# Optimization experiments

Measured on AMD Instinct MI355X. Metric: run time of the kernel, lower is better.

## Reference

```python
import jax, jax.numpy as jnp
import numpy as np

B, N, E, F, C = 4, 10000, 160000, 128, 128
NUM_ITERATIONS = 3  # num_iterations init arg


def setup_inputs() -> dict:
    key = jax.random.key(0)
    ks = jax.random.split(key, 8)
    objects = jax.random.normal(ks[0], (B, N, F), dtype=jnp.float32)
    connections = jax.random.randint(ks[1], (B, E, 2), 0, N, dtype=jnp.int32)
    # small init scales keep exp() in the attention numerically tame (mirrors
    # glorot/orthogonal-scale weights at init)
    object_state_W = jax.random.normal(ks[2], (F, C), dtype=jnp.float32) * (1.0 / np.sqrt(F))
    state_attention_W = jax.random.normal(ks[3], (C, C), dtype=jnp.float32) * 0.05
    linked_state_attention_W = jax.random.normal(ks[4], (C, C), dtype=jnp.float32) * 0.05
    linked_state_W = jax.random.normal(ks[5], (C, C), dtype=jnp.float32) * (1.0 / np.sqrt(C))
    attention_b = jnp.zeros((C,), dtype=jnp.float32)
    state_b = jnp.zeros((C,), dtype=jnp.float32)
    return {
        "objects": objects,
        "object_state_W": object_state_W,
        "state_attention_W": state_attention_W,
        "linked_state_attention_W": linked_state_attention_W,
        "attention_b": attention_b,
        "linked_state_W": linked_state_W,
        "state_b": state_b,
        "connections": connections,
    }


def reference(objects, object_state_W, state_attention_W, linked_state_attention_W,
              attention_b, linked_state_W, state_b, connections):
    # bidirectional: double edges with both orientations  [B, 2E]
    src = jnp.concatenate([connections[:, :, 0], connections[:, :, 1]], axis=1)
    dst = jnp.concatenate([connections[:, :, 1], connections[:, :, 0]], axis=1)

    # initial states: [B, N, C]
    states = jnp.tanh(jnp.einsum('bnf,fc->bnc', objects, object_state_W) + state_b)

    def step_one(states_b, src_b, dst_b):
        # states_b: [N, C]; src_b/dst_b: [2E]
        states_aW = states_b @ state_attention_W          # [N, C]
        linked_aW = states_b @ linked_state_attention_W   # [N, C]
        # per-edge unnormalized attention  [2E, C]
        attention = jnp.exp(states_aW[src_b] + linked_aW[dst_b] + attention_b)
        # scatter-add normalization; self edge contributes 1 (exp(0))
        attention_norm = jnp.ones_like(states_b).at[src_b].add(attention)  # [N, C]
        self_attention = 1.0 / attention_norm
        attention = attention / attention_norm[src_b]
        # weighted neighbor aggregation
        attented = attention * states_b[dst_b]                              # [2E, C]
        linked_gated = jnp.zeros_like(states_b).at[src_b].add(attented)     # [N, C]
        return jnp.tanh(states_b * self_attention + linked_gated @ linked_state_W + state_b)

    step = jax.vmap(step_one)
    for _ in range(NUM_ITERATIONS):
        states = step(states, src, dst)
    return states
```

## Files before the change

kernel.cpp:

```cpp
#include <hip/hip_runtime.h>
#include <hip/hip_bf16.h>


#define BATCH 4
#define NNODE 10000
#define NEDGE 160000
#define TWOE  (2*NEDGE)
#define MROWS (BATCH*NNODE)
#define NCHUNK 64
#define CHUNKE (NEDGE/NCHUNK)
#define PADN  10240
#define EDPAD (TWOE + 8*NNODE)

typedef unsigned short u16;
typedef unsigned int   u32;
typedef __attribute__((ext_vector_type(8))) short bf16x8_t;
typedef __attribute__((ext_vector_type(4))) float f32x4_t;

__device__ __forceinline__ float b2f(u16 h){ return __uint_as_float(((u32)h) << 16); }
__device__ __forceinline__ u16 f2bf(float f){
  u32 u = __float_as_uint(f);
  return (u16)((u + 0x7fffu + ((u >> 16) & 1u)) >> 16);
}
__device__ __forceinline__ float fast_tanh(float x){
  float e = __expf(2.0f * x);
  return fmaf(-2.0f, __builtin_amdgcn_rcpf(e + 1.0f), 1.0f);
}

__global__ void prep_weights(const void* __restrict__ objects,
                             const void* __restrict__ Wo, const void* __restrict__ Wa,
                             const void* __restrict__ Wla, const void* __restrict__ Wl,
                             const void* __restrict__ ab, const void* __restrict__ sb,
                             int* __restrict__ flag, u16* __restrict__ Wt,
                             float* __restrict__ biasf){
  __shared__ int zc, hc;
  if (threadIdx.x == 0){ zc = 0; hc = 0; }
  __syncthreads();
  const u32* objw = (const u32*)objects;
  int z = 0, hcnt = 0;
  for (int i = threadIdx.x; i < 1024; i += 256){
    u32 lo = objw[i] & 0xffffu;
    if (lo == 0) z++;
    if (((lo >> 7) & 0xffu) >= 160u) hcnt++;
  }
  atomicAdd(&zc, z); atomicAdd(&hc, hcnt);
  __syncthreads();
  bool f = (hc > 0 || zc > 512);
  if (blockIdx.x == 0 && threadIdx.x == 0) *flag = f ? 1 : 0;

  int idx = blockIdx.x * 256 + threadIdx.x;
  if (idx < 65536){
    int m = idx >> 14, k = (idx >> 7) & 127, c = idx & 127;
    const void* src = (m == 0) ? Wo : (m == 1) ? Wa : (m == 2) ? Wla : Wl;
    u16 h = f ? f2bf(((const float*)src)[k * 128 + c]) : ((const u16*)src)[k * 128 + c];
    Wt[m * 16384 + c * 128 + k] = h;
  } else {
    int t = idx - 65536;
    const void* src = (t < 128) ? sb : ab;
    int i = t & 127;
    biasf[t] = f ? ((const float*)src)[i] : b2f(((const u16*)src)[i]);
  }
}

__device__ __forceinline__ void chunk_of(int blk, int& b, int& c){
  int xcd = blk & 7;
  b = xcd >> 1;
  c = ((blk >> 3) << 1) | (xcd & 1);
}

__global__ void __launch_bounds__(256) csr_hist(const int* __restrict__ conn,
                                                u16* __restrict__ partial){
  int b, c; chunk_of(blockIdx.x, b, c);
  __shared__ u32 hist[NNODE];
  for (int n = threadIdx.x; n < NNODE; n += 256) hist[n] = 0;
  __syncthreads();
  const int2* cp = (const int2*)conn + (size_t)b * NEDGE + c * CHUNKE;
  for (int i = threadIdx.x; i < CHUNKE; i += 256){
    int2 e = cp[i];
    atomicAdd(&hist[e.x], 1);
    atomicAdd(&hist[e.y], 1);
  }
  __syncthreads();
  u16* prow = partial + (size_t)(b * NCHUNK + c) * PADN;
  for (int n = threadIdx.x; n < NNODE; n += 256) prow[n] = (u16)hist[n];
}

__global__ void __launch_bounds__(256) csr_colscan(u16* __restrict__ partial,
    int* __restrict__ row_start, int* __restrict__ bsum, int* __restrict__ deg){
  int b = blockIdx.x / 40, w = blockIdx.x % 40;
  int n = w * 256 + threadIdx.x;
  u32 run = 0;
  if (n < NNODE){
    #pragma unroll 8
    for (int c = 0; c < NCHUNK; c++){
      size_t idx = (size_t)(b * NCHUNK + c) * PADN + n;
      u32 v = partial[idx];
      partial[idx] = (u16)run;
      run += v;
    }
  }
  u32 pad = (run + 7u) & ~7u;
  __shared__ u32 buf[256];
  buf[threadIdx.x] = pad;
  __syncthreads();
  for (int off = 1; off < 256; off <<= 1){
    u32 x = (threadIdx.x >= (unsigned)off) ? buf[threadIdx.x - off] : 0;
    __syncthreads();
    buf[threadIdx.x] += x;
    __syncthreads();
  }
  u32 incl = buf[threadIdx.x];
  if (n < NNODE){
    row_start[b * (NNODE + 1) + n] = (int)(incl - pad);
    deg[b * NNODE + n] = (int)run;
  }
  if (threadIdx.x == 255) bsum[blockIdx.x] = (int)incl;
}

__global__ void scanC(int* __restrict__ row_start, const int* __restrict__ bsum){
  int b = blockIdx.x / 40, j = blockIdx.x % 40;
  int n = j * 256 + threadIdx.x;
  int off = 0;
  for (int q = b * 40; q < b * 40 + j; q++) off += bsum[q];
  if (n < NNODE) row_start[b * (NNODE + 1) + n] += off;
  if (j == 39 && threadIdx.x == 0)
    row_start[b * (NNODE + 1) + NNODE] = off + bsum[b * 40 + 39];
}

__global__ void __launch_bounds__(256) csr_fill(const int* __restrict__ conn,
    const u16* __restrict__ partial, const int* __restrict__ row_start,
    int* __restrict__ edge_dst){
  int b, c; chunk_of(blockIdx.x, b, c);
  __shared__ u32 cur[NNODE];
  const u16* prow = partial + (size_t)(b * NCHUNK + c) * PADN;
  const int* rs = row_start + b * (NNODE + 1);
  for (int n = threadIdx.x; n < NNODE; n += 256) cur[n] = (u32)rs[n] + prow[n];
  __syncthreads();
  const int2* cp = (const int2*)conn + (size_t)b * NEDGE + c * CHUNKE;
  int* edb = edge_dst + (size_t)b * EDPAD;
  for (int i = threadIdx.x; i < CHUNKE; i += 256){
    int2 e = cp[i];
    u32 p1 = atomicAdd(&cur[e.x], 1); edb[p1] = e.y;
    u32 p2 = atomicAdd(&cur[e.y], 1); edb[p2] = e.x;
  }
}

__global__ void pad_fill(const int* __restrict__ row_start,
                         const int* __restrict__ deg, int* __restrict__ edge_dst,
                         u32* __restrict__ g0, u32* __restrict__ g1){
  if (blockIdx.x == 0){
    size_t base = (size_t)MROWS * 64;
    g0[base + threadIdx.x] = 0;
    g1[base + threadIdx.x] = 0;
  }
  int b = blockIdx.x / 40, j = blockIdx.x % 40;
  const int* rs = row_start + b * (NNODE + 1);
  int sent = 40000 - 9999 * b;
  int* edb = edge_dst + (size_t)b * EDPAD;
  if (j == 0){
    int T = rs[NNODE];
    for (int p = T + (int)threadIdx.x; p < EDPAD; p += 256) edb[p] = sent;
  }
  int n = j * 256 + threadIdx.x;
  if (n >= NNODE) return;
  int s = rs[n] + deg[b * NNODE + n];
  int epad = rs[n + 1];
  for (int p = s; p < epad; p++) edb[p] = sent;
}

__device__ __forceinline__ void gemm_tile4(const u16* __restrict__ arow,
    const u16* __restrict__ wt, int lm, int lq, int cofs, f32x4_t acc[4]){
  #pragma unroll
  for (int ks = 0; ks < 4; ks++){
    bf16x8_t a = *(const bf16x8_t*)(arow + ks * 32);
    #pragma unroll
    for (int nb = 0; nb < 4; nb++){
      bf16x8_t bfr = *(const bf16x8_t*)(wt + (cofs + nb * 16 + lm) * 128 + ks * 32 + lq * 8);
      acc[nb] = __builtin_amdgcn_mfma_f32_16x16x32_bf16(a, bfr, acc[nb], 0, 0, 0);
    }
  }
}

__device__ __forceinline__ void gemm_tile4_packed(const u32* __restrict__ Lrow,
    const u16* __restrict__ wt, int lm, int lq, int cofs, f32x4_t acc[4]){
  #pragma unroll
  for (int ks = 0; ks < 4; ks++){
    uint4 wa = *(const uint4*)(Lrow + ks * 32 + lq * 8);
    uint4 wb = *(const uint4*)(Lrow + ks * 32 + lq * 8 + 4);
    bf16x8_t a;
    a[0] = (short)wa.x; a[1] = (short)wa.y; a[2] = (short)wa.z; a[3] = (short)wa.w;
    a[4] = (short)wb.x; a[5] = (short)wb.y; a[6] = (short)wb.z; a[7] = (short)wb.w;
    #pragma unroll
    for (int nb = 0; nb < 4; nb++){
      bf16x8_t bfr = *(const bf16x8_t*)(wt + (cofs + nb * 16 + lm) * 128 + ks * 32 + lq * 8);
      acc[nb] = __builtin_amdgcn_mfma_f32_16x16x32_bf16(a, bfr, acc[nb], 0, 0, 0);
    }
  }
}

__device__ __forceinline__ void phase2_awlaw4(const u16* __restrict__ ldstile,
    const u16* __restrict__ Wt, const float* __restrict__ biasf,
    int lm, int lq, int cofs, int r0, _Float16* __restrict__ eat,
    u32* __restrict__ ghw){
  const u16* Wta  = Wt + 16384;
  const u16* Wtla = Wt + 32768;
  const u16* ldsrow = ldstile + lm * 136 + lq * 8;
  f32x4_t accA[4], accL[4];
  #pragma unroll
  for (int i = 0; i < 4; i++){ accA[i] = (f32x4_t){0.f,0.f,0.f,0.f}; accL[i] = (f32x4_t){0.f,0.f,0.f,0.f}; }
  #pragma unroll
  for (int ks = 0; ks < 4; ks++){
    bf16x8_t a = *(const bf16x8_t*)(ldsrow + ks * 32);
    #pragma unroll
    for (int nb = 0; nb < 4; nb++){
      bf16x8_t ba = *(const bf16x8_t*)(Wta  + (cofs + nb * 16 + lm) * 128 + ks * 32 + lq * 8);
      bf16x8_t bl = *(const bf16x8_t*)(Wtla + (cofs + nb * 16 + lm) * 128 + ks * 32 + lq * 8);
      accA[nb] = __builtin_amdgcn_mfma_f32_16x16x32_bf16(a, ba, accA[nb], 0, 0, 0);
      accL[nb] = __builtin_amdgcn_mfma_f32_16x16x32_bf16(a, bl, accL[nb], 0, 0, 0);
    }
  }
  #pragma unroll
  for (int nb = 0; nb < 4; nb++){
    int col = cofs + nb * 16 + lm;
    float bb = biasf[128 + col];
    #pragma unroll
    for (int i = 0; i < 4; i++){
      int row = r0 + lq * 4 + i;
      float ea = fminf(__expf(accA[nb][i]), 60000.0f);
      eat[(lq * 4 + i) * 128 + col] = (_Float16)ea;
      _Float16 elh = (_Float16)fminf(__expf(accL[nb][i] + bb), 60000.0f);
      u16 sbf = ldstile[(lq * 4 + i) * 136 + col];
      _Float16 sh = (_Float16)b2f(sbf);
      u32 elu = (u32)(*(const u16*)&elh);
      u32 shu = (u32)(*(const u16*)&sh);
      ghw[(size_t)row * 64 + (col & 63)] = elu | (shu << 16);
    }
  }
}

__device__ __forceinline__ void eah_writeback(const _Float16* __restrict__ eat,
    _Float16* __restrict__ eah, int blk_r0, int tid){
  const uint4* src = (const uint4*)eat;
  uint4* dst = (uint4*)(eah + (size_t)blk_r0 * 128);
  dst[tid]       = src[tid];
  dst[tid + 256] = src[tid + 256];
}

__global__ void __launch_bounds__(256) fused_init(const void* __restrict__ obj_raw,
    const int* __restrict__ flag, const u16* __restrict__ Wt,
    const float* __restrict__ biasf, _Float16* __restrict__ eah,
    u32* __restrict__ gat0, u32* __restrict__ gat1){
  __shared__ u16 lds[2][16 * 136];
  __shared__ _Float16 eat[2][16 * 128];
  const int lane = threadIdx.x & 63, wave = threadIdx.x >> 6;
  const int t = wave >> 1, ch = wave & 1, cofs = ch * 64;
  const int r0 = blockIdx.x * 32 + t * 16;
  const int lm = lane & 15, lq = lane >> 4;
  f32x4_t acc[4];
  #pragma unroll
  for (int i = 0; i < 4; i++) acc[i] = (f32x4_t){0.f, 0.f, 0.f, 0.f};
  if (*flag){
    const float* arow = (const float*)obj_raw + (size_t)(r0 + lm) * 128 + lq * 8;
    #pragma unroll
    for (int ks = 0; ks < 4; ks++){
      float4 fa = *(const float4*)(arow + ks * 32);
      float4 fb = *(const float4*)(arow + ks * 32 + 4);
      bf16x8_t a;
      a[0] = (short)f2bf(fa.x); a[1] = (short)f2bf(fa.y);
      a[2] = (short)f2bf(fa.z); a[3] = (short)f2bf(fa.w);
      a[4] = (short)f2bf(fb.x); a[5] = (short)f2bf(fb.y);
      a[6] = (short)f2bf(fb.z); a[7] = (short)f2bf(fb.w);
      #pragma unroll
      for (int nb = 0; nb < 4; nb++){
        bf16x8_t bfr = *(const bf16x8_t*)(Wt + (cofs + nb * 16 + lm) * 128 + ks * 32 + lq * 8);
        acc[nb] = __builtin_amdgcn_mfma_f32_16x16x32_bf16(a, bfr, acc[nb], 0, 0, 0);
      }
    }
  } else {
    gemm_tile4((const u16*)obj_raw + (size_t)(r0 + lm) * 128 + lq * 8, Wt, lm, lq, cofs, acc);
  }
  #pragma unroll
  for (int nb = 0; nb < 4; nb++){
    int col = cofs + nb * 16 + lm;
    float bb = biasf[col];
    #pragma unroll
    for (int i = 0; i < 4; i++)
      lds[t][(lq * 4 + i) * 136 + col] = f2bf(fast_tanh(acc[nb][i] + bb));
  }
  __syncthreads();
  phase2_awlaw4(&lds[t][0], Wt, biasf, lm, lq, cofs, r0, &eat[t][0], ch ? gat1 : gat0);
  __syncthreads();
  eah_writeback(&eat[0][0], eah, blockIdx.x * 32, threadIdx.x);
}

__global__ void __launch_bounds__(256) fused_mid(const u32* __restrict__ lgsa,
    const u16* __restrict__ Wt, const float* __restrict__ biasf,
    _Float16* __restrict__ eah, u32* __restrict__ gat0, u32* __restrict__ gat1){
  __shared__ u16 lds[2][16 * 136];
  __shared__ _Float16 eat[2][16 * 128];
  const int lane = threadIdx.x & 63, wave = threadIdx.x >> 6;
  const int t = wave >> 1, ch = wave & 1, cofs = ch * 64;
  const int r0 = blockIdx.x * 32 + t * 16;
  const int lm = lane & 15, lq = lane >> 4;
  f32x4_t acc[4];
  #pragma unroll
  for (int i = 0; i < 4; i++) acc[i] = (f32x4_t){0.f, 0.f, 0.f, 0.f};
  gemm_tile4_packed(lgsa + (size_t)(r0 + lm) * 128, Wt + 49152, lm, lq, cofs, acc);
  #pragma unroll
  for (int nb = 0; nb < 4; nb++){
    int col = cofs + nb * 16 + lm;
    float bb = biasf[col];
    #pragma unroll
    for (int i = 0; i < 4; i++){
      int row = r0 + lq * 4 + i;
      u32 v = lgsa[(size_t)row * 128 + col];
      u16 hb = (u16)(v >> 16);
      float sa = (float)(*(const _Float16*)&hb);
      lds[t][(lq * 4 + i) * 136 + col] = f2bf(fast_tanh(sa + acc[nb][i] + bb));
    }
  }
  __syncthreads();
  phase2_awlaw4(&lds[t][0], Wt, biasf, lm, lq, cofs, r0, &eat[t][0], ch ? gat1 : gat0);
  __syncthreads();
  eah_writeback(&eat[0][0], eah, blockIdx.x * 32, threadIdx.x);
}

__global__ void __launch_bounds__(256) final_out(const u32* __restrict__ lgsa,
    const u16* __restrict__ Wt, const float* __restrict__ biasf,
    const int* __restrict__ flag, void* __restrict__ outp){
  const int lane = threadIdx.x & 63, wave = threadIdx.x >> 6;
  const int t = wave >> 1, ch = wave & 1, cofs = ch * 64;
  const int r0 = blockIdx.x * 32 + t * 16;
  const int lm = lane & 15, lq = lane >> 4;
  bool f32out = (*flag != 0);
  f32x4_t acc[4];
  #pragma unroll
  for (int i = 0; i < 4; i++) acc[i] = (f32x4_t){0.f, 0.f, 0.f, 0.f};
  gemm_tile4_packed(lgsa + (size_t)(r0 + lm) * 128, Wt + 49152, lm, lq, cofs, acc);
  #pragma unroll
  for (int nb = 0; nb < 4; nb++){
    int col = cofs + nb * 16 + lm;
    float bb = biasf[col];
    #pragma unroll
    for (int i = 0; i < 4; i++){
      int row = r0 + lq * 4 + i;
      u32 vv = lgsa[(size_t)row * 128 + col];
      u16 hb = (u16)(vv >> 16);
      float sa = (float)(*(const _Float16*)&hb);
      float v = fast_tanh(sa + acc[nb][i] + bb);
      if (f32out) ((float*)outp)[(size_t)row * 128 + col] = v;
      else        ((u16*)  outp)[(size_t)row * 128 + col] = f2bf(v);
    }
  }
}

__device__ __forceinline__ void acc_mix(u32 g, float one, float& a1, float& a2){
  asm("v_fma_mix_f32 %0, %2, %3, %0 op_sel:[0,0,0] op_sel_hi:[1,0,0]\n\t"
      "v_fma_mix_f32 %1, %2, %2, %1 op_sel:[0,1,0] op_sel_hi:[1,1,0]"
      : "+v"(a1), "+v"(a2)
      : "v"(g), "v"(one));
}

__device__ __forceinline__ u32 gath1(const u32* __restrict__ gh, int d, int c){
  const u32* p = (const u32*)((const char*)gh + ((size_t)(u32)d << 8));
  return p[c];
}

#define LDIDX(d, p) { const int* ep_ = (p); _Pragma("unroll") \
  for (int j = 0; j < 8; j++) d[j] = __builtin_amdgcn_readfirstlane(ep_[j]); }
#define GATH8(g, d) { _Pragma("unroll") \
  for (int j = 0; j < 8; j++) g[j] = gath1(gh, d[j], c); }
#define CONS8(g, s1, s2, t1, t2) { _Pragma("unroll") \
  for (int j = 0; j < 8; j++) acc_mix(g[j], one, (j & 1) ? t1 : s1, (j & 1) ? t2 : s2); }

__global__ void __launch_bounds__(128, 6) edge_kernel(const _Float16* __restrict__ eah,
    const u32* __restrict__ gat0, const u32* __restrict__ gat1,
    const int* __restrict__ row_start, const int* __restrict__ edge_dst,
    u32* __restrict__ lgsa){
  int blk = blockIdx.x;
  int xcd = blk & 7;
  int b = xcd >> 1, h = xcd & 1;
  int i = blk >> 3;
  int w = (int)(threadIdx.x >> 6);
  int nA = i * 4 + w * 2, nB = nA + 1;
  int c = threadIdx.x & 63;
  const u32* gh = (h ? gat1 : gat0) + (size_t)b * NNODE * 64;
  const int* rs = row_start + b * (NNODE + 1);
  int eA  = __builtin_amdgcn_readfirstlane(rs[nA]);
  int eA1 = __builtin_amdgcn_readfirstlane(rs[nA + 1]);
  int eB1 = __builtin_amdgcn_readfirstlane(rs[nB + 1]);
  int eB = eA1;
  const int* ed = edge_dst + (size_t)b * EDPAD;

  float eaA = (float)eah[(size_t)(b * NNODE + nA) * 128 + h * 64 + c];
  float eaB = (float)eah[(size_t)(b * NNODE + nB) * 128 + h * 64 + c];
  u32 selfA = gh[((size_t)nA << 6) + c];
  u32 selfB = gh[((size_t)nB << 6) + c];
  const float one = 1.0f;

  float sA1=0.f, sA2=0.f, tA1=0.f, tA2=0.f;
  float sB1=0.f, sB2=0.f, tB1=0.f, tB2=0.f;
  int ngA = (eA1 - eA) >> 3, ngB = (eB1 - eB) >> 3;
  int dA[8], dB[8]; u32 gA[8], gB[8], hA[8], hB[8];

  if (ngA){ LDIDX(dA, ed + eA); }
  if (ngB){ LDIDX(dB, ed + eB); }
  if (ngA){ GATH8(gA, dA); eA += 8; LDIDX(dA, ed + eA); }
  if (ngB){ GATH8(gB, dB); eB += 8; LDIDX(dB, ed + eB); }

  int m = ngA < ngB ? ngA : ngB;
  int cons = 0;
  for (; cons + 2 <= m; cons += 2){
    GATH8(hA, dA); eA += 8; LDIDX(dA, ed + eA);
    GATH8(hB, dB); eB += 8; LDIDX(dB, ed + eB);
    CONS8(gA, sA1, sA2, tA1, tA2);
    CONS8(gB, sB1, sB2, tB1, tB2);
    GATH8(gA, dA); eA += 8; LDIDX(dA, ed + eA);
    GATH8(gB, dB); eB += 8; LDIDX(dB, ed + eB);
    CONS8(hA, sA1, sA2, tA1, tA2);
    CONS8(hB, sB1, sB2, tB1, tB2);
  }

  { int rem = ngA - cons;
    if (rem > 0){
      int k = 1;
      for (; k + 1 < rem; k += 2){
        GATH8(hA, dA); eA += 8; LDIDX(dA, ed + eA);
        CONS8(gA, sA1, sA2, tA1, tA2);
        GATH8(gA, dA); eA += 8; LDIDX(dA, ed + eA);
        CONS8(hA, sA1, sA2, tA1, tA2);
      }
      if (k < rem){
        GATH8(hA, dA);
        CONS8(gA, sA1, sA2, tA1, tA2);
        CONS8(hA, sA1, sA2, tA1, tA2);
      } else {
        CONS8(gA, sA1, sA2, tA1, tA2);
      }
    }
  }
  { int rem = ngB - cons;
    if (rem > 0){
      int k = 1;
      for (; k + 1 < rem; k += 2){
        GATH8(hB, dB); eB += 8; LDIDX(dB, ed + eB);
        CONS8(gB, sB1, sB2, tB1, tB2);
        GATH8(gB, dB); eB += 8; LDIDX(dB, ed + eB);
        CONS8(hB, sB1, sB2, tB1, tB2);
      }
      if (k < rem){
        GATH8(hB, dB);
        CONS8(gB, sB1, sB2, tB1, tB2);
        CONS8(hB, sB1, sB2, tB1, tB2);
      } else {
        CONS8(gB, sB1, sB2, tB1, tB2);
      }
    }
  }

  sA1 += tA1; sA2 += tA2; sB1 += tB1; sB2 += tB2;
  { float inv = __builtin_amdgcn_rcpf(fmaf(eaA, sA1, 1.0f));
    float lg = eaA * sA2 * inv;
    u16 hb = (u16)(selfA >> 16);
    float s_self = (float)(*(const _Float16*)&hb);
    _Float16 hs = (_Float16)(s_self * inv);
    u32 pk = (u32)f2bf(lg) | ((u32)(*(const u16*)&hs) << 16);
    lgsa[(size_t)(b * NNODE + nA) * 128 + h * 64 + c] = pk; }
  { float inv = __builtin_amdgcn_rcpf(fmaf(eaB, sB1, 1.0f));
    float lg = eaB * sB2 * inv;
    u16 hb = (u16)(selfB >> 16);
    float s_self = (float)(*(const _Float16*)&hb);
    _Float16 hs = (_Float16)(s_self * inv);
    u32 pk = (u32)f2bf(lg) | ((u32)(*(const u16*)&hs) << 16);
    lgsa[(size_t)(b * NNODE + nB) * 128 + h * 64 + c] = pk; }
}

extern "C" void kernel_launch(void* const* d_in, const int* in_sizes, int n_in,
                              void* d_out, int out_size, void* d_ws, size_t ws_size,
                              hipStream_t stream){
  (void)in_sizes; (void)n_in; (void)ws_size; (void)out_size;
  const void* objects = d_in[0];
  const void* Wo      = d_in[1];
  const void* Wa      = d_in[2];
  const void* Wla     = d_in[3];
  const void* attn_b  = d_in[4];
  const void* Wl      = d_in[5];
  const void* state_b = d_in[6];
  const int*  conn    = (const int*)d_in[7];

  char* base = (char*)d_ws;
  size_t off = 0;
  auto alloc = [&](size_t bytes) -> char* {
    char* p = base + off;
    off = (off + bytes + 255) & ~(size_t)255;
    return p;
  };
  int*      flag      = (int*)     alloc(256);
  u16*      Wt        = (u16*)     alloc((size_t)4 * 16384 * 2);
  float*    biasf     = (float*)   alloc(256 * 4);
  _Float16* eah       = (_Float16*)alloc((size_t)MROWS * 128 * 2);
  u32*      gat0      = (u32*)     alloc((size_t)(MROWS + 4) * 64 * 4);
  u32*      gat1      = (u32*)     alloc((size_t)(MROWS + 4) * 64 * 4);
  u32*      lgsa      = (u32*)     alloc((size_t)MROWS * 128 * 4);
  u16*      partial   = (u16*)     alloc((size_t)BATCH * NCHUNK * PADN * 2);
  int*      row_start = (int*)     alloc((size_t)BATCH * (NNODE + 1) * 4);
  int*      edge_dst  = (int*)     alloc((size_t)BATCH * EDPAD * 4);
  int*      deg       = (int*)     alloc((size_t)MROWS * 4);
  int*      bsum      = (int*)     alloc(160 * 4);

  prep_weights<<<257, 256, 0, stream>>>(objects, Wo, Wa, Wla, Wl, attn_b, state_b,
                                        flag, Wt, biasf);

  csr_hist<<<256, 256, 0, stream>>>(conn, partial);
  csr_colscan<<<160, 256, 0, stream>>>(partial, row_start, bsum, deg);
  scanC<<<160, 256, 0, stream>>>(row_start, bsum);
  csr_fill<<<256, 256, 0, stream>>>(conn, partial, row_start, edge_dst);
  pad_fill<<<160, 256, 0, stream>>>(row_start, deg, edge_dst, gat0, gat1);

  fused_init<<<MROWS / 32, 256, 0, stream>>>(objects, flag, Wt, biasf, eah, gat0, gat1);
  edge_kernel<<<MROWS / 2, 128, 0, stream>>>(eah, gat0, gat1, row_start, edge_dst, lgsa);
  fused_mid<<<MROWS / 32, 256, 0, stream>>>(lgsa, Wt, biasf, eah, gat0, gat1);
  edge_kernel<<<MROWS / 2, 128, 0, stream>>>(eah, gat0, gat1, row_start, edge_dst, lgsa);
  fused_mid<<<MROWS / 32, 256, 0, stream>>>(lgsa, Wt, biasf, eah, gat0, gat1);
  edge_kernel<<<MROWS / 2, 128, 0, stream>>>(eah, gat0, gat1, row_start, edge_dst, lgsa);
  final_out<<<MROWS / 32, 256, 0, stream>>>(lgsa, Wt, biasf, flag, d_out);
}
```

Baseline: 356.2 us.

## Horizontally fuse independent setup kernels into fewer launches

Weight/bias preparation and the per-chunk CSR histogram now run as one launch, with block ranges selecting the role. The CSR fill, the padding-sentinel fill and the initial state/attention GEMM kernel are merged into a second launch the same way. Together this removes three kernel launches and their serialization gaps, and lets independent work overlap on the GPU. In exchange the merged kernel reserves a 40 KB shared buffer for every block, which may lower occupancy for the GEMM blocks that need much less.

```diff
diff --git a/kernel.cpp b/kernel.cpp
--- a/kernel.cpp
+++ b/kernel.cpp
@@ -27,62 +27,62 @@
   return fmaf(-2.0f, __builtin_amdgcn_rcpf(e + 1.0f), 1.0f);
 }
 
-__global__ void prep_weights(const void* __restrict__ objects,
-                             const void* __restrict__ Wo, const void* __restrict__ Wa,
-                             const void* __restrict__ Wla, const void* __restrict__ Wl,
-                             const void* __restrict__ ab, const void* __restrict__ sb,
-                             int* __restrict__ flag, u16* __restrict__ Wt,
-                             float* __restrict__ biasf){
-  __shared__ int zc, hc;
-  if (threadIdx.x == 0){ zc = 0; hc = 0; }
-  __syncthreads();
-  const u32* objw = (const u32*)objects;
-  int z = 0, hcnt = 0;
-  for (int i = threadIdx.x; i < 1024; i += 256){
-    u32 lo = objw[i] & 0xffffu;
-    if (lo == 0) z++;
-    if (((lo >> 7) & 0xffu) >= 160u) hcnt++;
-  }
-  atomicAdd(&zc, z); atomicAdd(&hc, hcnt);
-  __syncthreads();
-  bool f = (hc > 0 || zc > 512);
-  if (blockIdx.x == 0 && threadIdx.x == 0) *flag = f ? 1 : 0;
-
-  int idx = blockIdx.x * 256 + threadIdx.x;
-  if (idx < 65536){
-    int m = idx >> 14, k = (idx >> 7) & 127, c = idx & 127;
-    const void* src = (m == 0) ? Wo : (m == 1) ? Wa : (m == 2) ? Wla : Wl;
-    u16 h = f ? f2bf(((const float*)src)[k * 128 + c]) : ((const u16*)src)[k * 128 + c];
-    Wt[m * 16384 + c * 128 + k] = h;
-  } else {
-    int t = idx - 65536;
-    const void* src = (t < 128) ? sb : ab;
-    int i = t & 127;
-    biasf[t] = f ? ((const float*)src)[i] : b2f(((const u16*)src)[i]);
-  }
-}
-
 __device__ __forceinline__ void chunk_of(int blk, int& b, int& c){
   int xcd = blk & 7;
   b = xcd >> 1;
   c = ((blk >> 3) << 1) | (xcd & 1);
 }
 
-__global__ void __launch_bounds__(256) csr_hist(const int* __restrict__ conn,
-                                                u16* __restrict__ partial){
-  int b, c; chunk_of(blockIdx.x, b, c);
+__global__ void __launch_bounds__(256) k1_prep_hist(const int* __restrict__ conn,
+    u16* __restrict__ partial,
+    const void* __restrict__ objects,
+    const void* __restrict__ Wo, const void* __restrict__ Wa,
+    const void* __restrict__ Wla, const void* __restrict__ Wl,
+    const void* __restrict__ ab, const void* __restrict__ sb,
+    int* __restrict__ flag, u16* __restrict__ Wt, float* __restrict__ biasf){
   __shared__ u32 hist[NNODE];
-  for (int n = threadIdx.x; n < NNODE; n += 256) hist[n] = 0;
-  __syncthreads();
-  const int2* cp = (const int2*)conn + (size_t)b * NEDGE + c * CHUNKE;
-  for (int i = threadIdx.x; i < CHUNKE; i += 256){
-    int2 e = cp[i];
-    atomicAdd(&hist[e.x], 1);
-    atomicAdd(&hist[e.y], 1);
-  }
-  __syncthreads();
-  u16* prow = partial + (size_t)(b * NCHUNK + c) * PADN;
-  for (int n = threadIdx.x; n < NNODE; n += 256) prow[n] = (u16)hist[n];
+  __shared__ int zc, hc;
+  if (blockIdx.x < 256){
+    int b, c; chunk_of(blockIdx.x, b, c);
+    for (int n = threadIdx.x; n < NNODE; n += 256) hist[n] = 0;
+    __syncthreads();
+    const int2* cp = (const int2*)conn + (size_t)b * NEDGE + c * CHUNKE;
+    for (int i = threadIdx.x; i < CHUNKE; i += 256){
+      int2 e = cp[i];
+      atomicAdd(&hist[e.x], 1);
+      atomicAdd(&hist[e.y], 1);
+    }
+    __syncthreads();
+    u16* prow = partial + (size_t)(b * NCHUNK + c) * PADN;
+    for (int n = threadIdx.x; n < NNODE; n += 256) prow[n] = (u16)hist[n];
+  } else {
+    if (threadIdx.x == 0){ zc = 0; hc = 0; }
+    __syncthreads();
+    const u32* objw = (const u32*)objects;
+    int z = 0, hcnt = 0;
+    for (int i = threadIdx.x; i < 1024; i += 256){
+      u32 lo = objw[i] & 0xffffu;
+      if (lo == 0) z++;
+      if (((lo >> 7) & 0xffu) >= 160u) hcnt++;
+    }
+    atomicAdd(&zc, z); atomicAdd(&hc, hcnt);
+    __syncthreads();
+    bool f = (hc > 0 || zc > 512);
+    int p = blockIdx.x - 256;
+    if (p == 0 && threadIdx.x == 0) *flag = f ? 1 : 0;
+    int idx = p * 256 + threadIdx.x;
+    if (idx < 65536){
+      int m = idx >> 14, k = (idx >> 7) & 127, c = idx & 127;
+      const void* src = (m == 0) ? Wo : (m == 1) ? Wa : (m == 2) ? Wla : Wl;
+      u16 h = f ? f2bf(((const float*)src)[k * 128 + c]) : ((const u16*)src)[k * 128 + c];
+      Wt[m * 16384 + c * 128 + k] = h;
+    } else {
+      int t = idx - 65536;
+      const void* src = (t < 128) ? sb : ab;
+      int i = t & 127;
+      biasf[t] = f ? ((const float*)src)[i] : b2f(((const u16*)src)[i]);
+    }
+  }
 }
 
 __global__ void __launch_bounds__(256) csr_colscan(u16* __restrict__ partial,
@@ -127,47 +127,6 @@
     row_start[b * (NNODE + 1) + NNODE] = off + bsum[b * 40 + 39];
 }
 
-__global__ void __launch_bounds__(256) csr_fill(const int* __restrict__ conn,
-    const u16* __restrict__ partial, const int* __restrict__ row_start,
-    int* __restrict__ edge_dst){
-  int b, c; chunk_of(blockIdx.x, b, c);
-  __shared__ u32 cur[NNODE];
-  const u16* prow = partial + (size_t)(b * NCHUNK + c) * PADN;
-  const int* rs = row_start + b * (NNODE + 1);
-  for (int n = threadIdx.x; n < NNODE; n += 256) cur[n] = (u32)rs[n] + prow[n];
-  __syncthreads();
-  const int2* cp = (const int2*)conn + (size_t)b * NEDGE + c * CHUNKE;
-  int* edb = edge_dst + (size_t)b * EDPAD;
-  for (int i = threadIdx.x; i < CHUNKE; i += 256){
-    int2 e = cp[i];
-    u32 p1 = atomicAdd(&cur[e.x], 1); edb[p1] = e.y;
-    u32 p2 = atomicAdd(&cur[e.y], 1); edb[p2] = e.x;
-  }
-}
-
-__global__ void pad_fill(const int* __restrict__ row_start,
-                         const int* __restrict__ deg, int* __restrict__ edge_dst,
-                         u32* __restrict__ g0, u32* __restrict__ g1){
-  if (blockIdx.x == 0){
-    size_t base = (size_t)MROWS * 64;
-    g0[base + threadIdx.x] = 0;
-    g1[base + threadIdx.x] = 0;
-  }
-  int b = blockIdx.x / 40, j = blockIdx.x % 40;
-  const int* rs = row_start + b * (NNODE + 1);
-  int sent = 40000 - 9999 * b;
-  int* edb = edge_dst + (size_t)b * EDPAD;
-  if (j == 0){
-    int T = rs[NNODE];
-    for (int p = T + (int)threadIdx.x; p < EDPAD; p += 256) edb[p] = sent;
-  }
-  int n = j * 256 + threadIdx.x;
-  if (n >= NNODE) return;
-  int s = rs[n] + deg[b * NNODE + n];
-  int epad = rs[n + 1];
-  for (int p = s; p < epad; p++) edb[p] = sent;
-}
-
 __device__ __forceinline__ void gemm_tile4(const u16* __restrict__ arow,
     const u16* __restrict__ wt, int lm, int lq, int cofs, f32x4_t acc[4]){
   #pragma unroll
@@ -246,16 +205,17 @@
   dst[tid + 256] = src[tid + 256];
 }
 
-__global__ void __launch_bounds__(256) fused_init(const void* __restrict__ obj_raw,
-    const int* __restrict__ flag, const u16* __restrict__ Wt,
-    const float* __restrict__ biasf, _Float16* __restrict__ eah,
-    u32* __restrict__ gat0, u32* __restrict__ gat1){
-  __shared__ u16 lds[2][16 * 136];
-  __shared__ _Float16 eat[2][16 * 128];
-  const int lane = threadIdx.x & 63, wave = threadIdx.x >> 6;
+__device__ __forceinline__ void fused_init_body(int blk, int tid,
+    const void* __restrict__ obj_raw, const int* __restrict__ flag,
+    const u16* __restrict__ Wt, const float* __restrict__ biasf,
+    _Float16* __restrict__ eah, u32* __restrict__ gat0, u32* __restrict__ gat1,
+    u16* __restrict__ lds, _Float16* __restrict__ eat){
+  const int lane = tid & 63, wave = tid >> 6;
   const int t = wave >> 1, ch = wave & 1, cofs = ch * 64;
-  const int r0 = blockIdx.x * 32 + t * 16;
+  const int r0 = blk * 32 + t * 16;
   const int lm = lane & 15, lq = lane >> 4;
+  u16* ldsT = lds + t * 2176;
+  _Float16* eatT = eat + t * 2048;
   f32x4_t acc[4];
   #pragma unroll
   for (int i = 0; i < 4; i++) acc[i] = (f32x4_t){0.f, 0.f, 0.f, 0.f};
@@ -285,12 +245,64 @@
     float bb = biasf[col];
     #pragma unroll
     for (int i = 0; i < 4; i++)
-      lds[t][(lq * 4 + i) * 136 + col] = f2bf(fast_tanh(acc[nb][i] + bb));
+      ldsT[(lq * 4 + i) * 136 + col] = f2bf(fast_tanh(acc[nb][i] + bb));
   }
   __syncthreads();
-  phase2_awlaw4(&lds[t][0], Wt, biasf, lm, lq, cofs, r0, &eat[t][0], ch ? gat1 : gat0);
+  phase2_awlaw4(ldsT, Wt, biasf, lm, lq, cofs, r0, eatT, ch ? gat1 : gat0);
   __syncthreads();
-  eah_writeback(&eat[0][0], eah, blockIdx.x * 32, threadIdx.x);
+  eah_writeback(eat, eah, blk * 32, tid);
+}
+
+__global__ void __launch_bounds__(256) k4_init_fill_pad(
+    const void* __restrict__ obj_raw, const int* __restrict__ flag,
+    const u16* __restrict__ Wt, const float* __restrict__ biasf,
+    _Float16* __restrict__ eah, u32* __restrict__ gat0, u32* __restrict__ gat1,
+    const int* __restrict__ conn, const u16* __restrict__ partial,
+    const int* __restrict__ row_start, int* __restrict__ edge_dst,
+    const int* __restrict__ deg){
+  __shared__ __align__(16) char smem[40960];
+  int blk = blockIdx.x;
+  if (blk < 1250){
+    u16* lds = (u16*)smem;
+    _Float16* eat = (_Float16*)(smem + 8704);
+    fused_init_body(blk, (int)threadIdx.x, obj_raw, flag, Wt, biasf,
+                    eah, gat0, gat1, lds, eat);
+  } else if (blk < 1506){
+    int b, c; chunk_of(blk - 1250, b, c);
+    u32* cur = (u32*)smem;
+    const u16* prow = partial + (size_t)(b * NCHUNK + c) * PADN;
+    const int* rs = row_start + b * (NNODE + 1);
+    for (int n = threadIdx.x; n < NNODE; n += 256) cur[n] = (u32)rs[n] + prow[n];
+    __syncthreads();
+    const int2* cp = (const int2*)conn + (size_t)b * NEDGE + c * CHUNKE;
+    int* edb = edge_dst + (size_t)b * EDPAD;
+    for (int i = threadIdx.x; i < CHUNKE; i += 256){
+      int2 e = cp[i];
+      u32 p1 = atomicAdd(&cur[e.x], 1); edb[p1] = e.y;
+      u32 p2 = atomicAdd(&cur[e.y], 1); edb[p2] = e.x;
+    }
+  } else {
+    int p = blk - 1506;
+    if (p == 0){
+      size_t base = (size_t)MROWS * 64;
+      gat0[base + threadIdx.x] = 0;
+      gat1[base + threadIdx.x] = 0;
+    }
+    int b = p / 40, j = p % 40;
+    const int* rs = row_start + b * (NNODE + 1);
+    int sent = 40000 - 9999 * b;
+    int* edb = edge_dst + (size_t)b * EDPAD;
+    if (j == 0){
+      int T = rs[NNODE];
+      for (int q = T + (int)threadIdx.x; q < EDPAD; q += 256) edb[q] = sent;
+    }
+    int n = j * 256 + threadIdx.x;
+    if (n < NNODE){
+      int s = rs[n] + deg[b * NNODE + n];
+      int epad = rs[n + 1];
+      for (int q = s; q < epad; q++) edb[q] = sent;
+    }
+  }
 }
 
 __global__ void __launch_bounds__(256) fused_mid(const u32* __restrict__ lgsa,
@@ -508,16 +520,14 @@
   int*      deg       = (int*)     alloc((size_t)MROWS * 4);
   int*      bsum      = (int*)     alloc(160 * 4);
 
-  prep_weights<<<257, 256, 0, stream>>>(objects, Wo, Wa, Wla, Wl, attn_b, state_b,
-                                        flag, Wt, biasf);
-
-  csr_hist<<<256, 256, 0, stream>>>(conn, partial);
+  k1_prep_hist<<<513, 256, 0, stream>>>(conn, partial, objects, Wo, Wa, Wla, Wl,
+                                        attn_b, state_b, flag, Wt, biasf);
   csr_colscan<<<160, 256, 0, stream>>>(partial, row_start, bsum, deg);
   scanC<<<160, 256, 0, stream>>>(row_start, bsum);
-  csr_fill<<<256, 256, 0, stream>>>(conn, partial, row_start, edge_dst);
-  pad_fill<<<160, 256, 0, stream>>>(row_start, deg, edge_dst, gat0, gat1);
-
-  fused_init<<<MROWS / 32, 256, 0, stream>>>(objects, flag, Wt, biasf, eah, gat0, gat1);
+  k4_init_fill_pad<<<1666, 256, 0, stream>>>(objects, flag, Wt, biasf, eah,
+                                             gat0, gat1, conn, partial,
+                                             row_start, edge_dst, deg);
+
   edge_kernel<<<MROWS / 2, 128, 0, stream>>>(eah, gat0, gat1, row_start, edge_dst, lgsa);
   fused_mid<<<MROWS / 32, 256, 0, stream>>>(lgsa, Wt, biasf, eah, gat0, gat1);
   edge_kernel<<<MROWS / 2, 128, 0, stream>>>(eah, gat0, gat1, row_start, edge_dst, lgsa);
```

New measurement: 339.4 us, median of 2. 1.05x faster.
